# Optimization experiments

Measured on AMD Instinct MI355X. Metric: run time of the kernel, lower is better.

Reference implementation:

```python
import jax, jax.numpy as jnp
import numpy as np

NUM_HEADS = 16


def setup_inputs() -> dict:
    key = jax.random.key(0)
    ks = jax.random.split(key, 4)
    B, S, H = 2, 2048, 1024
    hidden_states = jax.random.normal(ks[0], (B, S, H), dtype=jnp.float32)
    attention_mask = jnp.zeros((B, 1, 1, S), dtype=jnp.float32)
    scale = 1.0 / np.sqrt(H)
    Wq = jax.random.normal(ks[1], (H, H), dtype=jnp.float32) * scale
    Wk = jax.random.normal(ks[2], (H, H), dtype=jnp.float32) * scale
    Wv = jax.random.normal(ks[3], (H, H), dtype=jnp.float32) * scale
    bq = jnp.zeros((H,), dtype=jnp.float32)
    bk = jnp.zeros((H,), dtype=jnp.float32)
    bv = jnp.zeros((H,), dtype=jnp.float32)
    return {"hidden_states": hidden_states, "attention_mask": attention_mask,
            "Wq": Wq, "bq": bq, "Wk": Wk, "bk": bk, "Wv": Wv, "bv": bv}


def _split_heads(x, B, S):
    # [B, S, H] -> [B, h, S, d]
    return x.reshape(B, S, NUM_HEADS, -1).transpose(0, 2, 1, 3)


def reference(hidden_states, attention_mask, Wq, bq, Wk, bk, Wv, bv):
    B, S, H = hidden_states.shape
    d = H // NUM_HEADS
    q = _split_heads(hidden_states @ Wq + bq, B, S)  # [B,h,S,d]
    k = _split_heads(hidden_states @ Wk + bk, B, S)
    v = _split_heads(hidden_states @ Wv + bv, B, S)

    scores = jnp.einsum('bhqd,bhkd->bhqk', q, k) / jnp.sqrt(jnp.float32(d))
    # causal mask: -inf strictly above diagonal, plus additive pad mask
    i = jnp.arange(S)[:, None]
    j = jnp.arange(S)[None, :]
    causal = jnp.where(j > i, -jnp.inf, 0.0).astype(scores.dtype)  # [S,S]
    scores = scores + attention_mask + causal[None, None, :, :]

    probs = jax.nn.softmax(scores, axis=-1)  # dropout prob = 0.0 -> identity
    context = jnp.einsum('bhqk,bhkd->bhqd', probs, v)  # [B,h,S,d]
    return context.transpose(0, 2, 1, 3).reshape(B, S, H)
```

## Files before the change

### kernel.cpp

```cpp
#include <hip/hip_runtime.h>

typedef __attribute__((ext_vector_type(4)))  float f32x4;
typedef __attribute__((ext_vector_type(16))) float f32x16;
typedef __attribute__((ext_vector_type(8)))  short bf16x8;

typedef __attribute__((address_space(1))) const void gvoid;
typedef __attribute__((address_space(3))) void lvoid;

__device__ __forceinline__ void gl_lds16(const void* g, void* l) {
  __builtin_amdgcn_global_load_lds((gvoid*)g, (lvoid*)l, 16, 0, 0);
}

__device__ __forceinline__ float exp2_fast(float x) {
  return __builtin_amdgcn_exp2f(x);
}

__device__ __forceinline__ ushort f2bf(float f) {
  union { float f; unsigned u; } v; v.f = f;
  unsigned u = v.u;
  return (ushort)((u + 0x7fffu + ((u >> 16) & 1u)) >> 16);
}

__device__ __forceinline__ uint cvt_pk_bf16(float lo, float hi) {
  uint r;
  asm("v_cvt_pk_bf16_f32 %0, %1, %2" : "=v"(r) : "v"(lo), "v"(hi));
  return r;
}
__device__ __forceinline__ void plswap(uint& x, uint& y) {
  asm volatile("v_permlane32_swap_b32 %0, %1" : "+v"(x), "+v"(y));
}

__global__ __launch_bounds__(256) void cvt_x(const float* __restrict__ x,
                                             ushort* __restrict__ o) {
  int idx = blockIdx.x * 256 + threadIdx.x;
  float4 v = reinterpret_cast<const float4*>(x)[idx];
  ushort4 r;
  r.x = f2bf(v.x); r.y = f2bf(v.y); r.z = f2bf(v.z); r.w = f2bf(v.w);
  reinterpret_cast<ushort4*>(o)[idx] = r;
}

__global__ __launch_bounds__(256) void wtrans(const float* __restrict__ Wq,
                                              const float* __restrict__ Wk,
                                              const float* __restrict__ Wv,
                                              ushort* __restrict__ WT) {
  __shared__ ushort tile[64 * 68];
  int bx = blockIdx.x;
  int w = bx >> 8, rem = bx & 255;
  int k0 = (rem >> 4) << 6, n0 = (rem & 15) << 6;
  const float* W = (w == 0) ? Wq : (w == 1) ? Wk : Wv;
  int tid = threadIdx.x;
#pragma unroll
  for (int it = 0; it < 4; ++it) {
    int idx = tid + it * 256;
    int r = idx >> 4, c4 = (idx & 15) * 4;
    float4 v = *reinterpret_cast<const float4*>(&W[(k0 + r) * 1024 + n0 + c4]);
    ushort4 u;
    u.x = f2bf(v.x); u.y = f2bf(v.y); u.z = f2bf(v.z); u.w = f2bf(v.w);
    *reinterpret_cast<ushort4*>(&tile[r * 68 + c4]) = u;
  }
  __syncthreads();
#pragma unroll
  for (int it = 0; it < 4; ++it) {
    int idx = tid + it * 256;
    int n = idx >> 4, k4 = (idx & 15) * 4;
    ushort4 o;
    o.x = tile[(k4 + 0) * 68 + n];
    o.y = tile[(k4 + 1) * 68 + n];
    o.z = tile[(k4 + 2) * 68 + n];
    o.w = tile[(k4 + 3) * 68 + n];
    *reinterpret_cast<ushort4*>(&WT[w * 1048576 + (size_t)(n0 + n) * 1024 + k0 + k4]) = o;
  }
}

__global__ __launch_bounds__(256) void qkv_gemm(
    const ushort* __restrict__ Xb, const ushort* __restrict__ WT,
    const float* __restrict__ bq, const float* __restrict__ bk,
    const float* __restrict__ bv, ushort* __restrict__ Qb,
    ushort* __restrict__ Kb, ushort* __restrict__ VT) {
  __shared__ ushort smem[128 * 136];
  ushort* Xs = smem;
  ushort* Ws = smem + 8192;
  int tid = threadIdx.x;
  int wave = tid >> 6, lane = tid & 63, g = lane >> 4, lr = lane & 15;
  int wr = wave >> 1, wc = wave & 1;
  int m0 = blockIdx.x << 7;
  int n0g = blockIdx.y << 7;
  f32x4 acc[4][4];
#pragma unroll
  for (int i = 0; i < 4; ++i)
#pragma unroll
    for (int j = 0; j < 4; ++j) { acc[i][j][0] = 0.f; acc[i][j][1] = 0.f; acc[i][j][2] = 0.f; acc[i][j][3] = 0.f; }

  int l3 = lane >> 3;
  int jsw = ((lane & 7) ^ l3) * 8;
  int swz = lr & 7;
  for (int k0 = 0; k0 < 1024; k0 += 64) {
    __syncthreads();
#pragma unroll
    for (int c = 0; c < 4; ++c) {
      int cw = wave * 4 + c;
      int row = cw * 8 + l3;
      gl_lds16(Xb + (size_t)(m0 + row) * 1024 + k0 + jsw, Xs + cw * 512);
      gl_lds16(WT + (size_t)(n0g + row) * 1024 + k0 + jsw, Ws + cw * 512);
    }
    __syncthreads();
#pragma unroll
    for (int ks = 0; ks < 2; ++ks) {
      bf16x8 a[4], b[4];
      int slot = ((ks * 4 + g) ^ swz) * 8;
#pragma unroll
      for (int mi = 0; mi < 4; ++mi)
        a[mi] = *reinterpret_cast<const bf16x8*>(&Xs[(wr * 64 + mi * 16 + lr) * 64 + slot]);
#pragma unroll
      for (int ni = 0; ni < 4; ++ni)
        b[ni] = *reinterpret_cast<const bf16x8*>(&Ws[(wc * 64 + ni * 16 + lr) * 64 + slot]);
#pragma unroll
      for (int mi = 0; mi < 4; ++mi)
#pragma unroll
        for (int ni = 0; ni < 4; ++ni)
          acc[mi][ni] = __builtin_amdgcn_mfma_f32_16x16x32_bf16(a[mi], b[ni], acc[mi][ni], 0, 0, 0);
    }
  }
  __syncthreads();

  int which = n0g >> 10;
  const float* bias = (which == 0) ? bq : (which == 1) ? bk : bv;
  int nloc0 = (n0g & 1023);
  if (which == 2) {
#pragma unroll
    for (int ni = 0; ni < 4; ++ni) {
      int row = wc * 64 + ni * 16 + lr;
      float bb = bias[nloc0 + row];
#pragma unroll
      for (int mi = 0; mi < 4; ++mi) {
        int m = wr * 64 + mi * 16 + g * 4;
        ushort4 v4;
        v4.x = f2bf(acc[mi][ni][0] + bb);
        v4.y = f2bf(acc[mi][ni][1] + bb);
        v4.z = f2bf(acc[mi][ni][2] + bb);
        v4.w = f2bf(acc[mi][ni][3] + bb);
        *reinterpret_cast<ushort4*>(&smem[row * 136 + m]) = v4;
      }
    }
    __syncthreads();
    int b_ = m0 >> 11, s0 = m0 & 2047;
#pragma unroll
    for (int it = 0; it < 8; ++it) {
      int c = tid + it * 256;
      int row = c >> 4, mc = (c & 15) * 8;
      uint4 vv = *reinterpret_cast<const uint4*>(&smem[row * 136 + mc]);
      int n = nloc0 + row;
      int hh = n >> 6, dd = n & 63;
      *reinterpret_cast<uint4*>(&VT[((size_t)(b_ * 16 + hh) * 64 + dd) * 2048 + s0 + mc]) = vv;
    }
  } else {
#pragma unroll
    for (int ni = 0; ni < 4; ++ni) {
      int n = wc * 64 + ni * 16 + lr;
      float bb = bias[nloc0 + n];
#pragma unroll
      for (int mi = 0; mi < 4; ++mi) {
#pragma unroll
        for (int r = 0; r < 4; ++r)
          smem[(wr * 64 + mi * 16 + g * 4 + r) * 136 + n] = f2bf(acc[mi][ni][r] + bb);
      }
    }
    __syncthreads();
    ushort* ob = (which == 0) ? Qb : Kb;
#pragma unroll
    for (int it = 0; it < 8; ++it) {
      int c = tid + it * 256;
      int row = c >> 4, nc = (c & 15) * 8;
      uint4 vv = *reinterpret_cast<const uint4*>(&smem[row * 136 + nc]);
      int m = m0 + row;
      int b_ = m >> 11, s = m & 2047;
      int n = nloc0 + nc;
      int hh = n >> 6, dd = n & 63;
      *reinterpret_cast<uint4*>(&ob[((size_t)(b_ * 16 + hh) * 2048 + s) * 64 + dd]) = vv;
    }
  }
}

__device__ __forceinline__ void softmax_state(f32x16& s, float& mrun, float& lrun,
                                              f32x16& Od0, f32x16& Od1,
                                              bf16x8& p0, bf16x8& p1) {
  float tmx = s[0];
#pragma unroll
  for (int j = 1; j < 16; ++j) tmx = fmaxf(tmx, s[j]);
  tmx = fmaxf(tmx, __shfl_xor(tmx, 32));
  if (!__all(tmx - mrun <= 11.5f)) {
    float nm = fmaxf(mrun, tmx);
    float al = exp2_fast(mrun - nm);
    mrun = nm;
    lrun *= al;
#pragma unroll
    for (int j = 0; j < 16; ++j) { Od0[j] *= al; Od1[j] *= al; }
  }
  float rs = 0.f;
#pragma unroll
  for (int j = 0; j < 16; ++j) { float p = exp2_fast(s[j] - mrun); s[j] = p; rs += p; }
  rs += __shfl_xor(rs, 32);
  lrun += rs;
  uint x0 = cvt_pk_bf16(s[0], s[1]),   y0 = cvt_pk_bf16(s[4], s[5]);
  uint x1 = cvt_pk_bf16(s[2], s[3]),   y1 = cvt_pk_bf16(s[6], s[7]);
  plswap(x0, y0); plswap(x1, y1);
  uint x2 = cvt_pk_bf16(s[8], s[9]),   y2 = cvt_pk_bf16(s[12], s[13]);
  uint x3 = cvt_pk_bf16(s[10], s[11]), y3 = cvt_pk_bf16(s[14], s[15]);
  plswap(x2, y2); plswap(x3, y3);
  union U { uint w[4]; bf16x8 v; } u0, u1;
  u0.w[0] = x0; u0.w[1] = x1; u0.w[2] = y0; u0.w[3] = y1;
  u1.w[0] = x2; u1.w[1] = x3; u1.w[2] = y2; u1.w[3] = y3;
  p0 = u0.v; p1 = u1.v;
}

__device__ __forceinline__ void attn_stage(const ushort* Kh, const ushort* VTh,
                                           const float* maskp, char* smem,
                                           int buf, int kv0, int tid, int jsw) {
  ushort* Ksb = (ushort*)(smem + buf * 16384);
  ushort* Vsb = Ksb + 4096;
  int wave = tid >> 6, lane = tid & 63;
  int l3 = lane >> 3;
#pragma unroll
  for (int c = 0; c < 4; ++c) {
    int ch = wave * 4 + c;
    int row = ch * 8 + l3;
    gl_lds16(Kh + (size_t)(kv0 + row) * 64 + jsw, Ksb + ch * 512);
    gl_lds16(VTh + (size_t)row * 2048 + kv0 + jsw, Vsb + ch * 512);
  }
  if (tid < 16) {
    float* Msb = (float*)(smem + 32768 + buf * 256);
    float4 m4 = *reinterpret_cast<const float4*>(maskp + kv0 + tid * 4);
    m4.x *= 1.44269504f; m4.y *= 1.44269504f; m4.z *= 1.44269504f; m4.w *= 1.44269504f;
    *reinterpret_cast<float4*>(Msb + tid * 4) = m4;
  }
}

__device__ __forceinline__ void attn_writeout(char* smem, int wave, int lane,
                                              const f32x16& Od0, const f32x16& Od1,
                                              float lrun, float* outp, int q0w) {
  float* Ot = (float*)smem + wave * 2176;
  int hi = lane >> 5, l31 = lane & 31;
  float rl = 1.0f / lrun;
#pragma unroll
  for (int jj = 0; jj < 4; ++jj) {
    int d0a = jj * 8 + 4 * hi;
    float4 w0, w1;
    w0.x = Od0[jj * 4 + 0] * rl; w0.y = Od0[jj * 4 + 1] * rl;
    w0.z = Od0[jj * 4 + 2] * rl; w0.w = Od0[jj * 4 + 3] * rl;
    w1.x = Od1[jj * 4 + 0] * rl; w1.y = Od1[jj * 4 + 1] * rl;
    w1.z = Od1[jj * 4 + 2] * rl; w1.w = Od1[jj * 4 + 3] * rl;
    *reinterpret_cast<float4*>(&Ot[l31 * 68 + d0a]) = w0;
    *reinterpret_cast<float4*>(&Ot[l31 * 68 + 32 + d0a]) = w1;
  }
  int qr = lane >> 1, half = lane & 1;
  const float* Orow = &Ot[qr * 68 + half * 32];
  float* og = outp + (size_t)(q0w + qr) * 1024 + half * 32;
#pragma unroll
  for (int c2 = 0; c2 < 8; ++c2)
    *reinterpret_cast<float4*>(og + c2 * 4) = *reinterpret_cast<const float4*>(Orow + c2 * 4);
}

__global__ __launch_bounds__(128) void attn(const ushort* __restrict__ Qb,
                                            const ushort* __restrict__ Kb,
                                            const ushort* __restrict__ VT,
                                            const float* __restrict__ mask,
                                            float* __restrict__ out) {
  __shared__ char smem[33280];
  const float SCALE = 0.125f * 1.44269504f;
  int tid = threadIdx.x;
  int wave = tid >> 6, lane = tid & 63;
  int hi = lane >> 5, l31 = lane & 31;
  int jsw = ((lane & 7) ^ (lane >> 3)) * 8;
  int pi = blockIdx.x & 15, bh = blockIdx.x >> 4;
  int b_ = bh >> 4, h = bh & 15;
  const ushort* Qh = Qb + (size_t)bh * 131072;
  const ushort* Kh = Kb + (size_t)bh * 131072;
  const ushort* VTh = VT + (size_t)bh * 131072;
  const float* maskp = mask + b_ * 2048;
  int qa0 = pi * 64 + wave * 32;
  int qb0 = (31 - pi) * 64 + wave * 32;
  int tmax = 31 - pi;

  bf16x8 aqa[4], aqb[4];
#pragma unroll
  for (int ds = 0; ds < 4; ++ds) {
    aqa[ds] = *reinterpret_cast<const bf16x8*>(Qh + (qa0 + l31) * 64 + ds * 16 + hi * 8);
    aqb[ds] = *reinterpret_cast<const bf16x8*>(Qh + (qb0 + l31) * 64 + ds * 16 + hi * 8);
  }

  f32x16 OA0, OA1, OB0, OB1;
#pragma unroll
  for (int j = 0; j < 16; ++j) { OA0[j] = 0.f; OA1[j] = 0.f; OB0[j] = 0.f; OB1[j] = 0.f; }
  float mA = -__builtin_inff(), lA = 0.f, mB = -__builtin_inff(), lB = 0.f;

  attn_stage(Kh, VTh, maskp, smem, 0, 0, tid, jsw);

  for (int t = 0; t <= tmax; ++t) {
    int cur = t & 1;
    __syncthreads();
    if (t < tmax) attn_stage(Kh, VTh, maskp, smem, cur ^ 1, (t + 1) << 6, tid, jsw);
    ushort* Ksb = (ushort*)(smem + cur * 16384);
    ushort* Vsb = Ksb + 4096;
    const float* Msb = (const float*)(smem + 32768 + cur * 256);
    int kv0 = t << 6;
#pragma unroll
    for (int sub = 0; sub < 2; ++sub) {
      int kvb = kv0 + sub * 32;
      bool actA = (kvb <= qa0), actB = (kvb <= qb0);
      if (!actB && !actA) continue;
      bf16x8 kf[4];
      int krow = sub * 32 + l31;
      int ksw = krow & 7;
#pragma unroll
      for (int ds = 0; ds < 4; ++ds)
        kf[ds] = *reinterpret_cast<const bf16x8*>(Ksb + krow * 64 + (((ds * 2 + hi) ^ ksw) * 8));
      f32x16 sB, sA;
      __builtin_amdgcn_s_setprio(1);
      if (actB) {
#pragma unroll
        for (int j = 0; j < 16; ++j) sB[j] = 0.f;
#pragma unroll
        for (int ds = 0; ds < 4; ++ds)
          sB = __builtin_amdgcn_mfma_f32_32x32x16_bf16(kf[ds], aqb[ds], sB, 0, 0, 0);
      }
      if (actA) {
#pragma unroll
        for (int j = 0; j < 16; ++j) sA[j] = 0.f;
#pragma unroll
        for (int ds = 0; ds < 4; ++ds)
          sA = __builtin_amdgcn_mfma_f32_32x32x16_bf16(kf[ds], aqa[ds], sA, 0, 0, 0);
      }
      __builtin_amdgcn_s_setprio(0);

      float4 mv[4];
#pragma unroll
      for (int jj = 0; jj < 4; ++jj)
        mv[jj] = *reinterpret_cast<const float4*>(Msb + sub * 32 + jj * 8 + 4 * hi);

      bf16x8 pB0, pB1, pA0, pA1;
      if (actB) {
        bool dg = (kvb == qb0);
#pragma unroll
        for (int jj = 0; jj < 4; ++jj) {
          const float* mvp = (const float*)&mv[jj];
#pragma unroll
          for (int r = 0; r < 4; ++r) {
            int j = jj * 4 + r;
            float v = sB[j] * SCALE + mvp[r];
            if (dg) {
              int kvg = kvb + jj * 8 + 4 * hi + r;
              v = (kvg > qb0 + l31) ? -__builtin_inff() : v;
            }
            sB[j] = v;
          }
        }
        softmax_state(sB, mB, lB, OB0, OB1, pB0, pB1);
      }
      if (actA) {
        bool dg = (kvb == qa0);
#pragma unroll
        for (int jj = 0; jj < 4; ++jj) {
          const float* mvp = (const float*)&mv[jj];
#pragma unroll
          for (int r = 0; r < 4; ++r) {
            int j = jj * 4 + r;
            float v = sA[j] * SCALE + mvp[r];
            if (dg) {
              int kvg = kvb + jj * 8 + 4 * hi + r;
              v = (kvg > qa0 + l31) ? -__builtin_inff() : v;
            }
            sA[j] = v;
          }
        }
        softmax_state(sA, mA, lA, OA0, OA1, pA0, pA1);
      }

      __builtin_amdgcn_s_setprio(1);
#pragma unroll
      for (int ks = 0; ks < 2; ++ks) {
#pragma unroll
        for (int h2 = 0; h2 < 2; ++h2) {
          int drow = h2 * 32 + l31;
          bf16x8 vf = *reinterpret_cast<const bf16x8*>(
              Vsb + drow * 64 + (((sub * 4 + ks * 2 + hi) ^ (drow & 7)) * 8));
          if (actB) {
            f32x16& O = h2 ? OB1 : OB0;
            O = __builtin_amdgcn_mfma_f32_32x32x16_bf16(vf, ks ? pB1 : pB0, O, 0, 0, 0);
          }
          if (actA) {
            f32x16& O = h2 ? OA1 : OA0;
            O = __builtin_amdgcn_mfma_f32_32x32x16_bf16(vf, ks ? pA1 : pA0, O, 0, 0, 0);
          }
        }
      }
      __builtin_amdgcn_s_setprio(0);
    }
  }

  __syncthreads();
  float* outp = out + (size_t)b_ * 2048 * 1024 + h * 64;
  attn_writeout(smem, wave, lane, OA0, OA1, lA, outp, qa0);
  attn_writeout(smem, wave, lane, OB0, OB1, lB, outp, qb0);
}

extern "C" void kernel_launch(void* const* d_in, const int* in_sizes, int n_in,
                              void* d_out, int out_size, void* d_ws, size_t ws_size,
                              hipStream_t stream) {
  const float* X    = (const float*)d_in[0];
  const float* mask = (const float*)d_in[1];
  const float* Wq   = (const float*)d_in[2];
  const float* bq   = (const float*)d_in[3];
  const float* Wk   = (const float*)d_in[4];
  const float* bk   = (const float*)d_in[5];
  const float* Wv   = (const float*)d_in[6];
  const float* bv   = (const float*)d_in[7];
  float* out = (float*)d_out;

  char* ws = (char*)d_ws;
  ushort* Xb  = (ushort*)ws;
  ushort* WTb = (ushort*)(ws + 8388608);
  ushort* Qb  = (ushort*)(ws + 8388608 + 6291456);
  ushort* Kb  = Qb + 4194304;
  ushort* VT  = Kb + 4194304;

  cvt_x<<<4096, 256, 0, stream>>>(X, Xb);
  wtrans<<<768, 256, 0, stream>>>(Wq, Wk, Wv, WTb);
  qkv_gemm<<<dim3(32, 24), 256, 0, stream>>>(Xb, WTb, bq, bk, bv, Qb, Kb, VT);
  attn<<<512, 128, 0, stream>>>(Qb, Kb, VT, mask, out);
}
```

Measured before the change: 224.6 us.

## Split KV tiles across two wave pairs per block and merge softmax partials

Doubles the attention block to 256 threads. Two wave pairs each process alternating KV tiles for the same query rows, with their own double-buffered LDS stages. At the end the partial outputs and max/sum statistics are combined through shared memory before writeout. It also remaps block indices so that neighbouring blocks cover different heads, and reads the mask directly from global memory instead of staging it in LDS. The aim is to shorten each block's serial KV loop. The cost is 64KB of LDS per block, which may limit occupancy, plus a final merge step.

```diff
diff --git a/kernel.cpp b/kernel.cpp
--- a/kernel.cpp
+++ b/kernel.cpp
@@ -213,25 +213,17 @@
   p0 = u0.v; p1 = u1.v;
 }
 
-__device__ __forceinline__ void attn_stage(const ushort* Kh, const ushort* VTh,
-                                           const float* maskp, char* smem,
-                                           int buf, int kv0, int tid, int jsw) {
+__device__ __forceinline__ void attn_stage2(const ushort* Kh, const ushort* VTh,
+                                            char* smem, int buf, int kv0,
+                                            int ws, int l3, int jsw) {
   ushort* Ksb = (ushort*)(smem + buf * 16384);
   ushort* Vsb = Ksb + 4096;
-  int wave = tid >> 6, lane = tid & 63;
-  int l3 = lane >> 3;
 #pragma unroll
   for (int c = 0; c < 4; ++c) {
-    int ch = wave * 4 + c;
+    int ch = ws * 4 + c;
     int row = ch * 8 + l3;
     gl_lds16(Kh + (size_t)(kv0 + row) * 64 + jsw, Ksb + ch * 512);
     gl_lds16(VTh + (size_t)row * 2048 + kv0 + jsw, Vsb + ch * 512);
-  }
-  if (tid < 16) {
-    float* Msb = (float*)(smem + 32768 + buf * 256);
-    float4 m4 = *reinterpret_cast<const float4*>(maskp + kv0 + tid * 4);
-    m4.x *= 1.44269504f; m4.y *= 1.44269504f; m4.z *= 1.44269504f; m4.w *= 1.44269504f;
-    *reinterpret_cast<float4*>(Msb + tid * 4) = m4;
   }
 }
 
@@ -260,26 +252,32 @@
     *reinterpret_cast<float4*>(og + c2 * 4) = *reinterpret_cast<const float4*>(Orow + c2 * 4);
 }
 
-__global__ __launch_bounds__(128) void attn(const ushort* __restrict__ Qb,
+__global__ __launch_bounds__(256) void attn(const ushort* __restrict__ Qb,
                                             const ushort* __restrict__ Kb,
                                             const ushort* __restrict__ VT,
                                             const float* __restrict__ mask,
                                             float* __restrict__ out) {
-  __shared__ char smem[33280];
+  __shared__ char smem[65536];
   const float SCALE = 0.125f * 1.44269504f;
+  const float L2E = 1.44269504f;
   int tid = threadIdx.x;
   int wave = tid >> 6, lane = tid & 63;
+  int strip = wave & 1, P = wave >> 1;
   int hi = lane >> 5, l31 = lane & 31;
-  int jsw = ((lane & 7) ^ (lane >> 3)) * 8;
-  int pi = blockIdx.x & 15, bh = blockIdx.x >> 4;
+  int l3 = lane >> 3;
+  int jsw = ((lane & 7) ^ l3) * 8;
+  int bid = blockIdx.x;
+  int logical = (bid & 7) * 64 + (bid >> 3);
+  int pi = logical & 15, bh = logical >> 4;
   int b_ = bh >> 4, h = bh & 15;
   const ushort* Qh = Qb + (size_t)bh * 131072;
   const ushort* Kh = Kb + (size_t)bh * 131072;
   const ushort* VTh = VT + (size_t)bh * 131072;
   const float* maskp = mask + b_ * 2048;
-  int qa0 = pi * 64 + wave * 32;
-  int qb0 = (31 - pi) * 64 + wave * 32;
+  int qa0 = pi * 64 + strip * 32;
+  int qb0 = (31 - pi) * 64 + strip * 32;
   int tmax = 31 - pi;
+  int nsup = (tmax + 2) >> 1;
 
   bf16x8 aqa[4], aqb[4];
 #pragma unroll
@@ -293,114 +291,161 @@
   for (int j = 0; j < 16; ++j) { OA0[j] = 0.f; OA1[j] = 0.f; OB0[j] = 0.f; OB1[j] = 0.f; }
   float mA = -__builtin_inff(), lA = 0.f, mB = -__builtin_inff(), lB = 0.f;
 
-  attn_stage(Kh, VTh, maskp, smem, 0, 0, tid, jsw);
-
-  for (int t = 0; t <= tmax; ++t) {
-    int cur = t & 1;
+  attn_stage2(Kh, VTh, smem, P, P << 6, strip, l3, jsw);
+
+  for (int s = 0; s < nsup; ++s) {
     __syncthreads();
-    if (t < tmax) attn_stage(Kh, VTh, maskp, smem, cur ^ 1, (t + 1) << 6, tid, jsw);
-    ushort* Ksb = (ushort*)(smem + cur * 16384);
-    ushort* Vsb = Ksb + 4096;
-    const float* Msb = (const float*)(smem + 32768 + cur * 256);
-    int kv0 = t << 6;
-#pragma unroll
-    for (int sub = 0; sub < 2; ++sub) {
-      int kvb = kv0 + sub * 32;
-      bool actA = (kvb <= qa0), actB = (kvb <= qb0);
-      if (!actB && !actA) continue;
-      bf16x8 kf[4];
-      int krow = sub * 32 + l31;
-      int ksw = krow & 7;
-#pragma unroll
-      for (int ds = 0; ds < 4; ++ds)
-        kf[ds] = *reinterpret_cast<const bf16x8*>(Ksb + krow * 64 + (((ds * 2 + hi) ^ ksw) * 8));
-      f32x16 sB, sA;
-      __builtin_amdgcn_s_setprio(1);
-      if (actB) {
-#pragma unroll
-        for (int j = 0; j < 16; ++j) sB[j] = 0.f;
+    int tn = 2 * (s + 1) + P;
+    if (tn <= tmax)
+      attn_stage2(Kh, VTh, smem, ((s + 1) & 1) * 2 + P, tn << 6, strip, l3, jsw);
+    int t = 2 * s + P;
+    if (t <= tmax) {
+      ushort* Ksb = (ushort*)(smem + ((s & 1) * 2 + P) * 16384);
+      ushort* Vsb = Ksb + 4096;
+      int kv0 = t << 6;
+#pragma unroll
+      for (int sub = 0; sub < 2; ++sub) {
+        int kvb = kv0 + sub * 32;
+        bool actA = (kvb <= qa0), actB = (kvb <= qb0);
+        if (!actB && !actA) continue;
+        bf16x8 kf[4];
+        int krow = sub * 32 + l31;
+        int ksw = krow & 7;
 #pragma unroll
         for (int ds = 0; ds < 4; ++ds)
-          sB = __builtin_amdgcn_mfma_f32_32x32x16_bf16(kf[ds], aqb[ds], sB, 0, 0, 0);
+          kf[ds] = *reinterpret_cast<const bf16x8*>(Ksb + krow * 64 + (((ds * 2 + hi) ^ ksw) * 8));
+        f32x16 sB, sA;
+        __builtin_amdgcn_s_setprio(1);
+        if (actB) {
+#pragma unroll
+          for (int j = 0; j < 16; ++j) sB[j] = 0.f;
+#pragma unroll
+          for (int ds = 0; ds < 4; ++ds)
+            sB = __builtin_amdgcn_mfma_f32_32x32x16_bf16(kf[ds], aqb[ds], sB, 0, 0, 0);
+        }
+        if (actA) {
+#pragma unroll
+          for (int j = 0; j < 16; ++j) sA[j] = 0.f;
+#pragma unroll
+          for (int ds = 0; ds < 4; ++ds)
+            sA = __builtin_amdgcn_mfma_f32_32x32x16_bf16(kf[ds], aqa[ds], sA, 0, 0, 0);
+        }
+        __builtin_amdgcn_s_setprio(0);
+
+        float4 mv[4];
+#pragma unroll
+        for (int jj = 0; jj < 4; ++jj) {
+          mv[jj] = *reinterpret_cast<const float4*>(maskp + kvb + jj * 8 + 4 * hi);
+          mv[jj].x *= L2E; mv[jj].y *= L2E; mv[jj].z *= L2E; mv[jj].w *= L2E;
+        }
+
+        bf16x8 pB0, pB1, pA0, pA1;
+        if (actB) {
+          bool dg = (kvb == qb0);
+#pragma unroll
+          for (int jj = 0; jj < 4; ++jj) {
+            const float* mvp = (const float*)&mv[jj];
+#pragma unroll
+            for (int r = 0; r < 4; ++r) {
+              int j = jj * 4 + r;
+              float v = sB[j] * SCALE + mvp[r];
+              if (dg) {
+                int kvg = kvb + jj * 8 + 4 * hi + r;
+                v = (kvg > qb0 + l31) ? -__builtin_inff() : v;
+              }
+              sB[j] = v;
+            }
+          }
+          softmax_state(sB, mB, lB, OB0, OB1, pB0, pB1);
+        }
+        if (actA) {
+          bool dg = (kvb == qa0);
+#pragma unroll
+          for (int jj = 0; jj < 4; ++jj) {
+            const float* mvp = (const float*)&mv[jj];
+#pragma unroll
+            for (int r = 0; r < 4; ++r) {
+              int j = jj * 4 + r;
+              float v = sA[j] * SCALE + mvp[r];
+              if (dg) {
+                int kvg = kvb + jj * 8 + 4 * hi + r;
+                v = (kvg > qa0 + l31) ? -__builtin_inff() : v;
+              }
+              sA[j] = v;
+            }
+          }
+          softmax_state(sA, mA, lA, OA0, OA1, pA0, pA1);
+        }
+
+        __builtin_amdgcn_s_setprio(1);
+#pragma unroll
+        for (int ks = 0; ks < 2; ++ks) {
+#pragma unroll
+          for (int h2 = 0; h2 < 2; ++h2) {
+            int drow = h2 * 32 + l31;
+            bf16x8 vf = *reinterpret_cast<const bf16x8*>(
+                Vsb + drow * 64 + (((sub * 4 + ks * 2 + hi) ^ (drow & 7)) * 8));
+            if (actB) {
+              f32x16& O = h2 ? OB1 : OB0;
+              O = __builtin_amdgcn_mfma_f32_32x32x16_bf16(vf, ks ? pB1 : pB0, O, 0, 0, 0);
+            }
+            if (actA) {
+              f32x16& O = h2 ? OA1 : OA0;
+              O = __builtin_amdgcn_mfma_f32_32x32x16_bf16(vf, ks ? pA1 : pA0, O, 0, 0, 0);
+            }
+          }
+        }
+        __builtin_amdgcn_s_setprio(0);
       }
-      if (actA) {
-#pragma unroll
-        for (int j = 0; j < 16; ++j) sA[j] = 0.f;
-#pragma unroll
-        for (int ds = 0; ds < 4; ++ds)
-          sA = __builtin_amdgcn_mfma_f32_32x32x16_bf16(kf[ds], aqa[ds], sA, 0, 0, 0);
+    }
+  }
+
+  __syncthreads();
+  float* mb = (float*)smem;
+  const int RS = 69;
+  if (P == 1) {
+    float* reg = mb + strip * (64 * RS) + lane * RS;
+#pragma unroll
+    for (int j = 0; j < 16; ++j) {
+      reg[j]      = OA0[j];
+      reg[16 + j] = OA1[j];
+      reg[32 + j] = OB0[j];
+      reg[48 + j] = OB1[j];
+    }
+    reg[64] = mA; reg[65] = lA; reg[66] = mB; reg[67] = lB;
+  }
+  __syncthreads();
+  if (P == 0) {
+    const float* reg = mb + strip * (64 * RS) + lane * RS;
+    {
+      float m2 = reg[64], l2 = reg[65];
+      float nm = fmaxf(mA, m2);
+      float a1 = exp2_fast(mA - nm), a2 = exp2_fast(m2 - nm);
+#pragma unroll
+      for (int j = 0; j < 16; ++j) {
+        OA0[j] = OA0[j] * a1 + reg[j] * a2;
+        OA1[j] = OA1[j] * a1 + reg[16 + j] * a2;
       }
-      __builtin_amdgcn_s_setprio(0);
-
-      float4 mv[4];
-#pragma unroll
-      for (int jj = 0; jj < 4; ++jj)
-        mv[jj] = *reinterpret_cast<const float4*>(Msb + sub * 32 + jj * 8 + 4 * hi);
-
-      bf16x8 pB0, pB1, pA0, pA1;
-      if (actB) {
-        bool dg = (kvb == qb0);
-#pragma unroll
-        for (int jj = 0; jj < 4; ++jj) {
-          const float* mvp = (const float*)&mv[jj];
-#pragma unroll
-          for (int r = 0; r < 4; ++r) {
-            int j = jj * 4 + r;
-            float v = sB[j] * SCALE + mvp[r];
-            if (dg) {
-              int kvg = kvb + jj * 8 + 4 * hi + r;
-              v = (kvg > qb0 + l31) ? -__builtin_inff() : v;
-            }
-            sB[j] = v;
-          }
-        }
-        softmax_state(sB, mB, lB, OB0, OB1, pB0, pB1);
+      lA = lA * a1 + l2 * a2; mA = nm;
+    }
+    {
+      float m2 = reg[66], l2 = reg[67];
+      float nm = fmaxf(mB, m2);
+      float a1 = exp2_fast(mB - nm), a2 = exp2_fast(m2 - nm);
+#pragma unroll
+      for (int j = 0; j < 16; ++j) {
+        OB0[j] = OB0[j] * a1 + reg[32 + j] * a2;
+        OB1[j] = OB1[j] * a1 + reg[48 + j] * a2;
       }
-      if (actA) {
-        bool dg = (kvb == qa0);
-#pragma unroll
-        for (int jj = 0; jj < 4; ++jj) {
-          const float* mvp = (const float*)&mv[jj];
-#pragma unroll
-          for (int r = 0; r < 4; ++r) {
-            int j = jj * 4 + r;
-            float v = sA[j] * SCALE + mvp[r];
-            if (dg) {
-              int kvg = kvb + jj * 8 + 4 * hi + r;
-              v = (kvg > qa0 + l31) ? -__builtin_inff() : v;
-            }
-            sA[j] = v;
-          }
-        }
-        softmax_state(sA, mA, lA, OA0, OA1, pA0, pA1);
-      }
-
-      __builtin_amdgcn_s_setprio(1);
-#pragma unroll
-      for (int ks = 0; ks < 2; ++ks) {
-#pragma unroll
-        for (int h2 = 0; h2 < 2; ++h2) {
-          int drow = h2 * 32 + l31;
-          bf16x8 vf = *reinterpret_cast<const bf16x8*>(
-              Vsb + drow * 64 + (((sub * 4 + ks * 2 + hi) ^ (drow & 7)) * 8));
-          if (actB) {
-            f32x16& O = h2 ? OB1 : OB0;
-            O = __builtin_amdgcn_mfma_f32_32x32x16_bf16(vf, ks ? pB1 : pB0, O, 0, 0, 0);
-          }
-          if (actA) {
-            f32x16& O = h2 ? OA1 : OA0;
-            O = __builtin_amdgcn_mfma_f32_32x32x16_bf16(vf, ks ? pA1 : pA0, O, 0, 0, 0);
-          }
-        }
-      }
-      __builtin_amdgcn_s_setprio(0);
-    }
-  }
-
+      lB = lB * a1 + l2 * a2; mB = nm;
+    }
+  }
   __syncthreads();
-  float* outp = out + (size_t)b_ * 2048 * 1024 + h * 64;
-  attn_writeout(smem, wave, lane, OA0, OA1, lA, outp, qa0);
-  attn_writeout(smem, wave, lane, OB0, OB1, lB, outp, qb0);
+  if (P == 0) {
+    float* outp = out + (size_t)b_ * 2048 * 1024 + h * 64;
+    attn_writeout(smem, wave, lane, OA0, OA1, lA, outp, qa0);
+    attn_writeout(smem, wave, lane, OB0, OB1, lB, outp, qb0);
+  }
 }
 
 extern "C" void kernel_launch(void* const* d_in, const int* in_sizes, int n_in,
@@ -426,5 +471,5 @@
   cvt_x<<<4096, 256, 0, stream>>>(X, Xb);
   wtrans<<<768, 256, 0, stream>>>(Wq, Wk, Wv, WTb);
   qkv_gemm<<<dim3(32, 24), 256, 0, stream>>>(Xb, WTb, bq, bk, bv, Qb, Kb, VT);
-  attn<<<512, 128, 0, stream>>>(Qb, Kb, VT, mask, out);
-}
+  attn<<<512, 256, 0, stream>>>(Qb, Kb, VT, mask, out);
+}
```

Result: slower. 229.9 us (+2.4%).
